# Kernel optimization log

Measured on AMD Instinct MI355X. Metric: run time of the kernel, lower is better.

Reference implementation:

```python
import jax, jax.numpy as jnp
import numpy as np

EMBED_DIM = 1024
N_HEADS = 16
HEAD_DIM = EMBED_DIM // N_HEADS

def setup_inputs() -> dict:
    key = jax.random.key(0)
    kx, kq, kk, kv, ko = jax.random.split(key, 5)
    s = 1.0 / np.sqrt(EMBED_DIM)
    return {
        "x": jax.random.normal(kx, (4, 2048, EMBED_DIM), dtype=jnp.float32),
        "Wq": jax.random.normal(kq, (EMBED_DIM, EMBED_DIM), dtype=jnp.float32) * s,
        "Wk": jax.random.normal(kk, (EMBED_DIM, EMBED_DIM), dtype=jnp.float32) * s,
        "Wv": jax.random.normal(kv, (EMBED_DIM, EMBED_DIM), dtype=jnp.float32) * s,
        "Wo": jax.random.normal(ko, (EMBED_DIM, EMBED_DIM), dtype=jnp.float32) * s,
    }

def reference(x, Wq, Wk, Wv, Wo):
    B, T, D = x.shape
    H, Dh = N_HEADS, HEAD_DIM
    # projections (nn.Linear: y = x @ W.T); split heads -> [B, H, T, Dh]
    Q = (x @ Wq.T).reshape(B, T, H, Dh).transpose(0, 2, 1, 3)
    K = (x @ Wk.T).reshape(B, T, H, Dh).transpose(0, 2, 1, 3)
    V = (x @ Wv.T).reshape(B, T, H, Dh).transpose(0, 2, 1, 3)
    scores = jnp.einsum("bhqd,bhkd->bhqk", Q, K) / jnp.sqrt(jnp.float32(Dh))
    attn = jax.nn.softmax(scores, axis=-1)
    out = jnp.einsum("bhqk,bhkd->bhqd", attn, V)  # [B,H,T,Dh]
    out = out.transpose(0, 2, 1, 3).reshape(B, T, D)
    return out @ Wo.T
```

## Files before the change

kernel.cpp:

```cpp
#include <hip/hip_runtime.h>

typedef _Float16 f16;
typedef _Float16 f16x8 __attribute__((ext_vector_type(8)));
typedef _Float16 f16x4 __attribute__((ext_vector_type(4)));
typedef float f32x4 __attribute__((ext_vector_type(4)));

#define MFMA16(a, b, c) __builtin_amdgcn_mfma_f32_16x16x32_f16((a), (b), (c), 0, 0, 0)
#define MEMBAR() __asm__ __volatile__("" ::: "memory")

__device__ __forceinline__ void cp16(const f16* g, f16* l) {
  __builtin_amdgcn_global_load_lds(
      (const __attribute__((address_space(1))) void*)g,
      (__attribute__((address_space(3))) void*)l, 16, 0, 0);
}

__global__ __launch_bounds__(256) void cvt_kernel(const float* __restrict__ src,
                                                  f16* __restrict__ dst) {
  int i = blockIdx.x * 256 + threadIdx.x;
  const float4* s = (const float4*)src;
  float4 a = s[2 * (size_t)i], b = s[2 * (size_t)i + 1];
  f16x8 o;
  o[0] = (f16)a.x; o[1] = (f16)a.y; o[2] = (f16)a.z; o[3] = (f16)a.w;
  o[4] = (f16)b.x; o[5] = (f16)b.y; o[6] = (f16)b.z; o[7] = (f16)b.w;
  *(f16x8*)(dst + (size_t)i * 8) = o;
}

__global__ __launch_bounds__(256) void cvtw_kernel(
    const float* __restrict__ s0, const float* __restrict__ s1,
    const float* __restrict__ s2, const float* __restrict__ s3,
    f16* __restrict__ d0, f16* __restrict__ d1,
    f16* __restrict__ d2, f16* __restrict__ d3) {
  int z = blockIdx.z;
  const float* src = (z == 0) ? s0 : (z == 1) ? s1 : (z == 2) ? s2 : s3;
  f16* dst = (z == 0) ? d0 : (z == 1) ? d1 : (z == 2) ? d2 : d3;
  int i = blockIdx.x * 256 + threadIdx.x;
  const float4* s = (const float4*)src;
  float4 a = s[2 * (size_t)i], b = s[2 * (size_t)i + 1];
  f16x8 o;
  o[0] = (f16)a.x; o[1] = (f16)a.y; o[2] = (f16)a.z; o[3] = (f16)a.w;
  o[4] = (f16)b.x; o[5] = (f16)b.y; o[6] = (f16)b.z; o[7] = (f16)b.w;
  *(f16x8*)(dst + (size_t)i * 8) = o;
}

template <bool OUT_F16>
__global__ __launch_bounds__(256, 2) void gemm_nt(
    const f16* __restrict__ A,
    const f16* __restrict__ B0, const f16* __restrict__ B1,
    void* __restrict__ C0, void* __restrict__ C1,
    int N, int K, float s0, float s1) {
  const int z = blockIdx.z;
  const f16* B = z ? B1 : B0;
  void* Cv = z ? C1 : C0;
  const float scale = z ? s1 : s0;
  __shared__ __align__(16) f16 As[8192];
  __shared__ __align__(16) f16 Bs[8192];
  const int tid = threadIdx.x;
  const int lane = tid & 63, w = tid >> 6;
  const int wm = w >> 1, wn = w & 1;
  const int c = lane & 15, q = lane >> 4;
  const int cx = c & 7;
  const size_t bm = blockIdx.y * 128, bn = blockIdx.x * 128;
  f32x4 acc[4][4] = {};

  for (int k0 = 0; k0 < K; k0 += 64) {
#pragma unroll
    for (int j = 0; j < 4; ++j) {
      int cb = (w * 4 + j) * 64;
      int ch = cb + lane;
      int row = ch >> 3, p = (ch & 7) ^ (row & 7);
      cp16(A + (bm + row) * (size_t)K + k0 + p * 8, As + cb * 8);
      cp16(B + (bn + row) * (size_t)K + k0 + p * 8, Bs + cb * 8);
    }
    __syncthreads();
#pragma unroll
    for (int kh = 0; kh < 2; ++kh) {
      f16x8 af[4], bf[4];
#pragma unroll
      for (int mt = 0; mt < 4; ++mt)
        af[mt] = *(const f16x8*)(As + (wm * 64 + mt * 16 + c) * 64 + ((kh * 4 + q) ^ cx) * 8);
#pragma unroll
      for (int nt = 0; nt < 4; ++nt)
        bf[nt] = *(const f16x8*)(Bs + (wn * 64 + nt * 16 + c) * 64 + ((kh * 4 + q) ^ cx) * 8);
#pragma unroll
      for (int mt = 0; mt < 4; ++mt)
#pragma unroll
        for (int nt = 0; nt < 4; ++nt)
          acc[mt][nt] = MFMA16(af[mt], bf[nt], acc[mt][nt]);
    }
    __syncthreads();
  }

#pragma unroll
  for (int mt = 0; mt < 4; ++mt)
#pragma unroll
    for (int nt = 0; nt < 4; ++nt)
#pragma unroll
      for (int r = 0; r < 4; ++r) {
        size_t row = bm + wm * 64 + mt * 16 + q * 4 + r;
        size_t col = bn + wn * 64 + nt * 16 + c;
        float v = acc[mt][nt][r] * scale;
        if constexpr (OUT_F16) ((f16*)Cv)[row * N + col] = (f16)v;
        else ((float*)Cv)[row * N + col] = v;
      }
}

__global__ __launch_bounds__(256, 4) void attn_kernel(
    const f16* __restrict__ Qg, const f16* __restrict__ Kg,
    const f16* __restrict__ VTg, f16* __restrict__ Og) {
  const int T = 2048, D = 1024;
  const int x = blockIdx.x;
  const int xcd = x & 7, rem = x >> 3;
  const int qt = rem & 15, grp = rem >> 4;
  const int bh = (grp << 3) | xcd;
  const int b = bh >> 4, h = bh & 15;
  const size_t base = ((size_t)b * T) * D + h * 64;
  const size_t baseV = (size_t)h * 64 * 8192 + (size_t)b * T;
  __shared__ __align__(16) f16 smem[20480];
  const int tid = threadIdx.x;
  const int lane = tid & 63, w = tid >> 6;
  const int c = lane & 15, q = lane >> 4;
  const int cx = c & 7;
  f16* Kb = smem;
  f16* Vb = smem + 8192;
  f16* Ps = smem + 16384 + w * 1024;

#pragma unroll
  for (int j = 0; j < 4; ++j) {
    int cb = (w * 4 + j) * 64;
    int ch = cb + lane;
    int row = ch >> 3, p = (ch & 7) ^ (row & 7);
    cp16(Qg + base + (size_t)(qt * 128 + row) * D + p * 8, smem + cb * 8);
  }
  __syncthreads();
  f16x8 qf[2][2];
#pragma unroll
  for (int nt = 0; nt < 2; ++nt)
#pragma unroll
    for (int kh = 0; kh < 2; ++kh)
      qf[nt][kh] = *(const f16x8*)(smem + (w * 32 + nt * 16 + c) * 64 + ((kh * 4 + q) ^ cx) * 8);
  __syncthreads();

  float l_[2] = {0.f, 0.f};
  f32x4 o_[2][4] = {};

  auto stageKV = [&](int kv, int bufi) {
    f16* Ks = Kb + bufi * 4096;
    f16* Vt = Vb + bufi * 4096;
#pragma unroll
    for (int j = 0; j < 2; ++j) {
      int cb = (w * 2 + j) * 64;
      int ch = cb + lane;
      int row = ch >> 3, p = (ch & 7) ^ (row & 7);
      cp16(Kg + base + (size_t)(kv + row) * D + p * 8, Ks + cb * 8);
    }
#pragma unroll
    for (int j = 0; j < 2; ++j) {
      int cb = (w * 2 + j) * 64;
      int ch = cb + lane;
      int row = ch >> 3, p = (ch & 7) ^ (row & 7);
      cp16(VTg + baseV + (size_t)row * 8192 + kv + p * 8, Vt + cb * 8);
    }
  };

  stageKV(0, 0);
  for (int i = 0; i < 32; ++i) {
    if (i < 31) {
      stageKV((i + 1) * 64, (i + 1) & 1);
      __builtin_amdgcn_s_waitcnt(0x0F74);
    } else {
      __builtin_amdgcn_s_waitcnt(0x0F70);
    }
    __builtin_amdgcn_s_barrier();
    f16* Ks = Kb + (i & 1) * 4096;
    f16* Vt = Vb + (i & 1) * 4096;

    f32x4 st[4][2] = {};
#pragma unroll
    for (int kh = 0; kh < 2; ++kh) {
      f16x8 kf[4];
#pragma unroll
      for (int mt = 0; mt < 4; ++mt)
        kf[mt] = *(const f16x8*)(Ks + (mt * 16 + c) * 64 + ((kh * 4 + q) ^ cx) * 8);
#pragma unroll
      for (int mt = 0; mt < 4; ++mt)
#pragma unroll
        for (int g = 0; g < 2; ++g)
          st[mt][g] = MFMA16(kf[mt], qf[g][kh], st[mt][g]);
    }

#pragma unroll
    for (int g = 0; g < 2; ++g) {
      float s = 0.f;
#pragma unroll
      for (int mt = 0; mt < 4; ++mt) {
        float p0 = __builtin_amdgcn_exp2f(st[mt][g][0]);
        float p1 = __builtin_amdgcn_exp2f(st[mt][g][1]);
        float p2 = __builtin_amdgcn_exp2f(st[mt][g][2]);
        float p3 = __builtin_amdgcn_exp2f(st[mt][g][3]);
        s += (p0 + p1) + (p2 + p3);
        f16x4 pv;
        pv[0] = (f16)p0; pv[1] = (f16)p1; pv[2] = (f16)p2; pv[3] = (f16)p3;
        *(f16x4*)(Ps + c * 64 + ((mt * 2 + (q >> 1)) ^ cx) * 8 + (q & 1) * 4) = pv;
      }
      s += __shfl_xor(s, 16);
      s += __shfl_xor(s, 32);
      l_[g] += s;

      MEMBAR();
#pragma unroll
      for (int kc = 0; kc < 2; ++kc) {
        f16x8 pf = *(const f16x8*)(Ps + c * 64 + ((kc * 4 + q) ^ cx) * 8);
#pragma unroll
        for (int d = 0; d < 4; ++d) {
          f16x8 vf = *(const f16x8*)(Vt + (d * 16 + c) * 64 + ((kc * 4 + q) ^ cx) * 8);
          o_[g][d] = MFMA16(pf, vf, o_[g][d]);
        }
      }
      MEMBAR();
    }
    __builtin_amdgcn_s_barrier();
  }

#pragma unroll
  for (int g = 0; g < 2; ++g)
#pragma unroll
    for (int r = 0; r < 4; ++r) {
      float linv = 1.0f / __shfl(l_[g], q * 4 + r);
      size_t row = (size_t)qt * 128 + w * 32 + g * 16 + q * 4 + r;
#pragma unroll
      for (int d = 0; d < 4; ++d)
        Og[base + row * D + d * 16 + c] = (f16)(o_[g][d][r] * linv);
    }
}

extern "C" void kernel_launch(void* const* d_in, const int* in_sizes, int n_in,
                              void* d_out, int out_size, void* d_ws, size_t ws_size,
                              hipStream_t stream) {
  const float* x  = (const float*)d_in[0];
  const float* Wq = (const float*)d_in[1];
  const float* Wk = (const float*)d_in[2];
  const float* Wv = (const float*)d_in[3];
  const float* Wo = (const float*)d_in[4];
  char* ws = (char*)d_ws;
  const size_t MB = 1ull << 20;
  f16* X16  = (f16*)(ws + 0 * MB);
  f16* Wq16 = (f16*)(ws + 16 * MB);
  f16* Wk16 = (f16*)(ws + 18 * MB);
  f16* Wv16 = (f16*)(ws + 20 * MB);
  f16* Wo16 = (f16*)(ws + 22 * MB);
  f16* Q16  = (f16*)(ws + 24 * MB);
  f16* K16  = (f16*)(ws + 40 * MB);
  f16* VT16 = (f16*)(ws + 56 * MB);
  f16* A16  = (f16*)(ws + 72 * MB);

  const float cs = 0.18033688011112042f;

  cvt_kernel<<<4096, 256, 0, stream>>>(x, X16);
  cvtw_kernel<<<dim3(512, 1, 4), 256, 0, stream>>>(
      Wq, Wk, Wv, Wo, Wq16, Wk16, Wv16, Wo16);

  gemm_nt<true><<<dim3(8, 64, 2), 256, 0, stream>>>(
      X16, Wq16, Wk16, (void*)Q16, (void*)K16, 1024, 1024, cs, 1.0f);

  gemm_nt<true><<<dim3(64, 8, 1), 256, 0, stream>>>(
      Wv16, X16, X16, (void*)VT16, (void*)VT16, 8192, 1024, 1.0f, 1.0f);

  attn_kernel<<<dim3(1024, 1, 1), 256, 0, stream>>>(Q16, K16, VT16, A16);

  gemm_nt<false><<<dim3(8, 64, 1), 256, 0, stream>>>(
      A16, Wo16, Wo16, d_out, d_out, 1024, 1024, 1.0f, 1.0f);
}
```

Measured before the change: 294.2 us.

## Double-buffer GEMM loads, merge QKV GEMMs and conversion kernels into single launches

The GEMM core now uses a K-step of 32 with two LDS buffers, so the next tile's async global-to-LDS copy is issued before computing on the current one, synchronised with explicit waitcnt and barriers. The Q, K and V^T projections are merged into one launch and the two fp16 conversion kernels into one, which removes launches and tail effects. Occupancy hint rises from 2 to 4 blocks per CU. The smaller K-step doubles the number of barriers per tile, and the hand-coded waitcnt values must match the number of outstanding loads.

```diff
diff --git a/kernel.cpp b/kernel.cpp
--- a/kernel.cpp
+++ b/kernel.cpp
@@ -14,80 +14,83 @@
       (__attribute__((address_space(3))) void*)l, 16, 0, 0);
 }
 
-__global__ __launch_bounds__(256) void cvt_kernel(const float* __restrict__ src,
-                                                  f16* __restrict__ dst) {
-  int i = blockIdx.x * 256 + threadIdx.x;
-  const float4* s = (const float4*)src;
-  float4 a = s[2 * (size_t)i], b = s[2 * (size_t)i + 1];
+__global__ __launch_bounds__(256) void cvt_all(
+    const float* __restrict__ x,  const float* __restrict__ Wq,
+    const float* __restrict__ Wk, const float* __restrict__ Wv,
+    const float* __restrict__ Wo,
+    f16* __restrict__ X16, f16* __restrict__ Wq16, f16* __restrict__ Wk16,
+    f16* __restrict__ Wv16, f16* __restrict__ Wo16) {
+  int blk = blockIdx.x;
+  const float* src; f16* dst; size_t off;
+  if (blk < 4096) { src = x; dst = X16; off = (size_t)blk * 2048; }
+  else {
+    int t = blk - 4096, widx = t >> 9, loc = t & 511;
+    src = (widx == 0) ? Wq : (widx == 1) ? Wk : (widx == 2) ? Wv : Wo;
+    dst = (widx == 0) ? Wq16 : (widx == 1) ? Wk16 : (widx == 2) ? Wv16 : Wo16;
+    off = (size_t)loc * 2048;
+  }
+  size_t e = off + (size_t)threadIdx.x * 8;
+  const float4* s = (const float4*)(src + e);
+  float4 a = s[0], b = s[1];
   f16x8 o;
   o[0] = (f16)a.x; o[1] = (f16)a.y; o[2] = (f16)a.z; o[3] = (f16)a.w;
   o[4] = (f16)b.x; o[5] = (f16)b.y; o[6] = (f16)b.z; o[7] = (f16)b.w;
-  *(f16x8*)(dst + (size_t)i * 8) = o;
-}
-
-__global__ __launch_bounds__(256) void cvtw_kernel(
-    const float* __restrict__ s0, const float* __restrict__ s1,
-    const float* __restrict__ s2, const float* __restrict__ s3,
-    f16* __restrict__ d0, f16* __restrict__ d1,
-    f16* __restrict__ d2, f16* __restrict__ d3) {
-  int z = blockIdx.z;
-  const float* src = (z == 0) ? s0 : (z == 1) ? s1 : (z == 2) ? s2 : s3;
-  f16* dst = (z == 0) ? d0 : (z == 1) ? d1 : (z == 2) ? d2 : d3;
-  int i = blockIdx.x * 256 + threadIdx.x;
-  const float4* s = (const float4*)src;
-  float4 a = s[2 * (size_t)i], b = s[2 * (size_t)i + 1];
-  f16x8 o;
-  o[0] = (f16)a.x; o[1] = (f16)a.y; o[2] = (f16)a.z; o[3] = (f16)a.w;
-  o[4] = (f16)b.x; o[5] = (f16)b.y; o[6] = (f16)b.z; o[7] = (f16)b.w;
-  *(f16x8*)(dst + (size_t)i * 8) = o;
-}
-
-template <bool OUT_F16>
-__global__ __launch_bounds__(256, 2) void gemm_nt(
-    const f16* __restrict__ A,
-    const f16* __restrict__ B0, const f16* __restrict__ B1,
-    void* __restrict__ C0, void* __restrict__ C1,
-    int N, int K, float s0, float s1) {
-  const int z = blockIdx.z;
-  const f16* B = z ? B1 : B0;
-  void* Cv = z ? C1 : C0;
-  const float scale = z ? s1 : s0;
-  __shared__ __align__(16) f16 As[8192];
-  __shared__ __align__(16) f16 Bs[8192];
+  *(f16x8*)(dst + e) = o;
+}
+
+__device__ __forceinline__ void gemm_core(
+    const f16* __restrict__ A, const f16* __restrict__ B, void* __restrict__ Cv,
+    bool outF16, int N, int K, int bm, int bn, float scale, f16* As, f16* Bs) {
   const int tid = threadIdx.x;
   const int lane = tid & 63, w = tid >> 6;
   const int wm = w >> 1, wn = w & 1;
   const int c = lane & 15, q = lane >> 4;
-  const int cx = c & 7;
-  const size_t bm = blockIdx.y * 128, bn = blockIdx.x * 128;
+  const int key = (c >> 1) & 3;
   f32x4 acc[4][4] = {};
 
-  for (int k0 = 0; k0 < K; k0 += 64) {
-#pragma unroll
-    for (int j = 0; j < 4; ++j) {
-      int cb = (w * 4 + j) * 64;
-      int ch = cb + lane;
-      int row = ch >> 3, p = (ch & 7) ^ (row & 7);
-      cp16(A + (bm + row) * (size_t)K + k0 + p * 8, As + cb * 8);
-      cp16(B + (bn + row) * (size_t)K + k0 + p * 8, Bs + cb * 8);
-    }
-    __syncthreads();
-#pragma unroll
-    for (int kh = 0; kh < 2; ++kh) {
-      f16x8 af[4], bf[4];
-#pragma unroll
-      for (int mt = 0; mt < 4; ++mt)
-        af[mt] = *(const f16x8*)(As + (wm * 64 + mt * 16 + c) * 64 + ((kh * 4 + q) ^ cx) * 8);
+  const int Lrow = lane >> 2, Lp = (lane & 3) ^ ((lane >> 3) & 3);
+  auto stage = [&](int k0, int bufi) {
+#pragma unroll
+    for (int j = 0; j < 2; ++j) {
+      int r0 = (w * 2 + j) * 16;
+      cp16(A + (size_t)(bm + r0 + Lrow) * K + k0 + Lp * 8,
+           As + bufi * 4096 + r0 * 32 + lane * 8);
+    }
+#pragma unroll
+    for (int j = 0; j < 2; ++j) {
+      int r0 = (w * 2 + j) * 16;
+      cp16(B + (size_t)(bn + r0 + Lrow) * K + k0 + Lp * 8,
+           Bs + bufi * 4096 + r0 * 32 + lane * 8);
+    }
+  };
+
+  stage(0, 0);
+  const int NIT = K >> 5;
+  for (int i = 0; i < NIT; ++i) {
+    if (i + 1 < NIT) {
+      stage((i + 1) << 5, (i + 1) & 1);
+      __builtin_amdgcn_s_waitcnt(0x0F74);
+    } else {
+      __builtin_amdgcn_s_waitcnt(0x0F70);
+    }
+    __builtin_amdgcn_s_barrier();
+    MEMBAR();
+    const f16* Ab = As + (i & 1) * 4096;
+    const f16* Bb = Bs + (i & 1) * 4096;
+    f16x8 af[4], bf[4];
+#pragma unroll
+    for (int mt = 0; mt < 4; ++mt)
+      af[mt] = *(const f16x8*)(Ab + (wm * 64 + mt * 16 + c) * 32 + (q ^ key) * 8);
+#pragma unroll
+    for (int nt = 0; nt < 4; ++nt)
+      bf[nt] = *(const f16x8*)(Bb + (wn * 64 + nt * 16 + c) * 32 + (q ^ key) * 8);
+#pragma unroll
+    for (int mt = 0; mt < 4; ++mt)
 #pragma unroll
       for (int nt = 0; nt < 4; ++nt)
-        bf[nt] = *(const f16x8*)(Bs + (wn * 64 + nt * 16 + c) * 64 + ((kh * 4 + q) ^ cx) * 8);
-#pragma unroll
-      for (int mt = 0; mt < 4; ++mt)
-#pragma unroll
-        for (int nt = 0; nt < 4; ++nt)
-          acc[mt][nt] = MFMA16(af[mt], bf[nt], acc[mt][nt]);
-    }
-    __syncthreads();
+        acc[mt][nt] = MFMA16(af[mt], bf[nt], acc[mt][nt]);
+    MEMBAR();
+    __builtin_amdgcn_s_barrier();
   }
 
 #pragma unroll
@@ -99,9 +102,32 @@
         size_t row = bm + wm * 64 + mt * 16 + q * 4 + r;
         size_t col = bn + wn * 64 + nt * 16 + c;
         float v = acc[mt][nt][r] * scale;
-        if constexpr (OUT_F16) ((f16*)Cv)[row * N + col] = (f16)v;
+        if (outF16) ((f16*)Cv)[row * N + col] = (f16)v;
         else ((float*)Cv)[row * N + col] = v;
       }
+}
+
+__global__ __launch_bounds__(256, 4) void gemm_qkvt(
+    const f16* __restrict__ X, const f16* __restrict__ Wq,
+    const f16* __restrict__ Wk, const f16* __restrict__ Wv,
+    f16* __restrict__ Q, f16* __restrict__ Ko, f16* __restrict__ VT, float cs) {
+  __shared__ __align__(16) f16 As[8192], Bs[8192];
+  const int z = blockIdx.z, x = blockIdx.x;
+  if (z < 2) {
+    gemm_core(X, z ? Wk : Wq, z ? (void*)Ko : (void*)Q, true, 1024, 1024,
+              (x >> 3) * 128, (x & 7) * 128, z ? 1.0f : cs, As, Bs);
+  } else {
+    gemm_core(Wv, X, (void*)VT, true, 8192, 1024,
+              (x >> 6) * 128, (x & 63) * 128, 1.0f, As, Bs);
+  }
+}
+
+__global__ __launch_bounds__(256, 4) void gemm_o(
+    const f16* __restrict__ A, const f16* __restrict__ Wo, float* __restrict__ out) {
+  __shared__ __align__(16) f16 As[8192], Bs[8192];
+  const int x = blockIdx.x;
+  gemm_core(A, Wo, (void*)out, false, 1024, 1024,
+            (x >> 3) * 128, (x & 7) * 128, 1.0f, As, Bs);
 }
 
 __global__ __launch_bounds__(256, 4) void attn_kernel(
@@ -255,18 +281,13 @@
 
   const float cs = 0.18033688011112042f;
 
-  cvt_kernel<<<4096, 256, 0, stream>>>(x, X16);
-  cvtw_kernel<<<dim3(512, 1, 4), 256, 0, stream>>>(
-      Wq, Wk, Wv, Wo, Wq16, Wk16, Wv16, Wo16);
-
-  gemm_nt<true><<<dim3(8, 64, 2), 256, 0, stream>>>(
-      X16, Wq16, Wk16, (void*)Q16, (void*)K16, 1024, 1024, cs, 1.0f);
-
-  gemm_nt<true><<<dim3(64, 8, 1), 256, 0, stream>>>(
-      Wv16, X16, X16, (void*)VT16, (void*)VT16, 8192, 1024, 1.0f, 1.0f);
+  cvt_all<<<6144, 256, 0, stream>>>(x, Wq, Wk, Wv, Wo,
+                                    X16, Wq16, Wk16, Wv16, Wo16);
+
+  gemm_qkvt<<<dim3(512, 1, 3), 256, 0, stream>>>(
+      X16, Wq16, Wk16, Wv16, Q16, K16, VT16, cs);
 
   attn_kernel<<<dim3(1024, 1, 1), 256, 0, stream>>>(Q16, K16, VT16, A16);
 
-  gemm_nt<false><<<dim3(8, 64, 1), 256, 0, stream>>>(
-      A16, Wo16, Wo16, d_out, d_out, 1024, 1024, 1.0f, 1.0f);
-}
+  gemm_o<<<512, 256, 0, stream>>>(A16, Wo16, (float*)d_out);
+}
```

Result: no change. 292.2 us (-0.7%).
